# Kernel tuning notes

Hardware: AMD Instinct MI355X
Metric: run time of the kernel (lower is better)

The kernel has to match this reference:

```python
import jax, jax.numpy as jnp
import numpy as np

DYADIC_ORDER = 1
SIGMA = 1.0  # RBF static kernel bandwidth (concrete static_kernel for the abstract base)


def static_kernel(x, y):
    # RBF Gram matrix: K[i, j] = exp(-||x_i - y_j||^2 / (2 * sigma^2)); x:(Lx,d) y:(Ly,d)
    sq = (jnp.sum(x * x, axis=-1)[:, None]
          + jnp.sum(y * y, axis=-1)[None, :]
          - 2.0 * (x @ y.T))
    return jnp.exp(-sq / (2.0 * SIGMA ** 2))


def finite_diff(K, dyadic_order):
    # second mixed finite difference of the static kernel, refined on a dyadic grid
    diff = K[1:, 1:] + K[:-1, :-1] - K[1:, :-1] - K[:-1, 1:]
    n = 2 ** dyadic_order
    diff = jnp.repeat(jnp.repeat(diff, n, axis=0), n, axis=1) / float(n * n)
    return diff  # ((Lx-1)*n, (Ly-1)*n)


def solve_pde_final(A):
    """Solve the Goursat PDE recurrence on a (M+1, N+1) grid with boundary 1,
    k11 = (k10 + k01) * (1 + inc/2 + inc^2/12) - k00 * (1 - inc^2/12),
    via an anti-diagonal (wavefront) lax.scan. Returns K[M, N]."""
    M, N = A.shape
    # skew A so anti-diagonals become rows: Adiag[t, r] = A[r, t - r]
    t = jnp.arange(M + N - 1)[:, None]
    r = jnp.arange(M)[None, :]
    c = t - r
    Adiag = jnp.where((c >= 0) & (c < N), A[r, jnp.clip(c, 0, N - 1)], 0.0)

    ii = jnp.arange(M + 1)          # row index along a diagonal
    ones = jnp.ones(M + 1, A.dtype)
    ds = jnp.arange(2, M + N + 1)   # diagonal index d = i + j

    def step(carry, xs):
        prev2, prev1 = carry        # diagonals d-2, d-1 (entry i holds K[i, d'-i])
        Ad, d = xs
        zero = jnp.zeros((1,), A.dtype)
        inc = jnp.concatenate([zero, Ad])            # inc[i] = A[i-1, d-i-1]
        k10 = jnp.concatenate([zero, prev1[:-1]])    # K[i-1, j]
        k01 = prev1                                  # K[i, j-1]
        k00 = jnp.concatenate([zero, prev2[:-1]])    # K[i-1, j-1]
        k11 = (k10 + k01) * (1.0 + 0.5 * inc + inc * inc / 12.0) \
              - k00 * (1.0 - inc * inc / 12.0)
        jj = d - ii
        new = jnp.where((ii == 0) | (jj == 0), 1.0, k11)   # boundary condition = 1
        new = jnp.where((jj < 0) | (jj > N), 1.0, new)     # outside grid: keep inert
        return (prev1, new), None

    (_, last), _ = jax.lax.scan(step, (ones, ones), (Adiag, ds))
    return last[M]  # K[M, N] = pde_sol[-1, -1]


def sig_kernel_pair(x, y):
    K = static_kernel(x, y)
    A = finite_diff(K, DYADIC_ORDER)
    return solve_pde_final(A)


def batch_kernel(xs, ys):
    # xs: (Bx, Lx, d), ys: (By, Ly, d) -> (Bx, By) signature-kernel Gram matrix
    return jax.vmap(lambda x: jax.vmap(lambda y: sig_kernel_pair(x, y))(ys))(xs)


def setup_inputs() -> dict:
    key = jax.random.key(0)
    kx, ky = jax.random.split(key)
    xs = jax.random.normal(kx, (16, 128, 8), dtype=jnp.float32)
    ys = jax.random.normal(ky, (16, 128, 8), dtype=jnp.float32)
    return {"xs": xs, "ys": ys}


def reference(xs, ys):
    return batch_kernel(xs, ys)
```

## Files before the change

### kernel.cpp

```cpp
#include <hip/hip_runtime.h>


#define LX 128
#define D  8
#define NB 16
#define NBODY 190

__global__ __launch_bounds__(256)
void sigkernel_kernel(const float* __restrict__ xs,
                      const float* __restrict__ ys,
                      float* __restrict__ out)
{
    __shared__ float sx[LX][D + 1];
    __shared__ float sy[LX][D + 1];
    __shared__ float xsqv[LX];
    __shared__ float ysqv[LX];
    __shared__ float B[LX * LX];

    const int t  = threadIdx.x;
    const int bx = blockIdx.x;
    const int by = blockIdx.y;
    const float* xp = xs + bx * (LX * D);
    const float* yp = ys + by * (LX * D);

    for (int e = t; e < LX * D; e += 256) {
        sx[e >> 3][e & 7] = xp[e];
        sy[e >> 3][e & 7] = yp[e];
    }
    __syncthreads();

    if (t < LX) {
        float sxx = 0.f, syy = 0.f;
        #pragma unroll
        for (int k = 0; k < D; ++k) {
            sxx += sx[t][k] * sx[t][k];
            syy += sy[t][k] * sy[t][k];
        }
        xsqv[t] = sxx;
        ysqv[t] = syy;
    }
    __syncthreads();

    {
        const int j = t & 127;
        float yr[D];
        #pragma unroll
        for (int k = 0; k < D; ++k) yr[k] = sy[j][k];
        const float ysq = ysqv[j];
        #pragma unroll
        for (int c = 0; c < 64; ++c) {
            const int e = t + c * 256;
            const int i = e >> 7;
            float dot = 0.f;
            #pragma unroll
            for (int k = 0; k < D; ++k) dot += sx[i][k] * yr[k];
            const float sq = xsqv[i] + ysq - 2.0f * dot;
            B[e] = expf(-0.5f * sq);
        }
    }
    __syncthreads();

    {
        float rv[64];
        #pragma unroll
        for (int c = 0; c < 64; ++c) {
            const int idx = t + c * 256;
            if (idx < 127 * 127) {
                const int i = idx / 127;
                const int j = idx - i * 127;
                rv[c] = 0.25f * (B[(i + 1) * 128 + (j + 1)] + B[i * 128 + j]
                               - B[(i + 1) * 128 + j]       - B[i * 128 + (j + 1)]);
            }
        }
        __syncthreads();
        #pragma unroll
        for (int c = 0; c < 64; ++c) {
            const int idx = t + c * 256;
            if (idx < 127 * 127) {
                const int i = idx / 127;
                const int j = idx - i * 127;
                B[i * 128 + j] = rv[c];
            }
        }
        if (t < 127) B[t * 128 + 127] = 0.f;
    }
    __syncthreads();

    if (t >= 64) return;

    const int l = t;
    const int rowa = 2 * l;
    const int rowb = (2 * l + 1 > 126) ? 126 : 2 * l + 1;
    const int baseA = rowa * 128;
    const int baseB = rowb * 128;
    const bool lane0 = (l == 0);

    double cur0 = 1.0, cur1 = 1.0, cur2 = 1.0, cur3 = 1.0;
    double h0 = 1.0, h1 = 1.0, h2 = 1.0;

    float inA, inB;
    {
        const int q = -l;
        const bool cl = ((unsigned)q > 126u);
        inA = B[cl ? 127 : (baseA + q)];
        inB = B[cl ? 127 : (baseB + q)];
    }

    for (int k = 0; k < NBODY; ++k) {
        const double ia = (double)inA;
        const double ib = (double)inB;
        const double ea = ia * ia * (1.0 / 12.0);
        const double eb = ib * ib * (1.0 / 12.0);
        const double c1a = 1.0 + 0.5 * ia + ea, c2a = 1.0 - ea;
        const double c1b = 1.0 + 0.5 * ib + eb, c2b = 1.0 - eb;

        {
            const int qn = k + 1 - l;
            const bool cl = ((unsigned)qn > 126u);
            inA = B[cl ? 127 : (baseA + qn)];
            inB = B[cl ? 127 : (baseB + qn)];
        }

        #pragma unroll
        for (int sub = 0; sub < 2; ++sub) {
            const double k10 = lane0 ? 1.0 : h1;
            const double k00 = lane0 ? 1.0 : h2;
            const double n0 = (k10 + cur0) * c1a - k00  * c2a;
            const double n1 = (n0  + cur1) * c1a - cur0 * c2a;
            const double n2 = (n1  + cur2) * c1b - cur1 * c2b;
            const double n3 = (n2  + cur3) * c1b - cur2 * c2b;
            cur0 = n0; cur1 = n1; cur2 = n2; cur3 = n3;
            const double sh = __shfl_up(n3, 1);
            h2 = h1; h1 = h0; h0 = sh;
        }
    }

    if (l == 63) out[bx * NB + by] = (float)cur1;
}

extern "C" void kernel_launch(void* const* d_in, const int* in_sizes, int n_in,
                              void* d_out, int out_size, void* d_ws, size_t ws_size,
                              hipStream_t stream)
{
    const float* xs = (const float*)d_in[0];
    const float* ys = (const float*)d_in[1];
    float* out = (float*)d_out;
    dim3 grid(NB, NB);
    dim3 block(256);
    hipLaunchKernelGGL(sigkernel_kernel, grid, block, 0, stream, xs, ys, out);
}
```

Baseline: 89.48 us.

## Switch PDE wavefront recurrence to fp32 and simplify finite-difference indexing

Runs the serial Goursat wavefront recurrence in single precision instead of double. Fp64 work is replaced by fp32 FMAs, and each shuffle moves one 32-bit register instead of a 64-bit pair. The finite-difference pass now indexes linearly with a padded shared buffer, which removes the per-element divide by 127. The lane-0 boundary select moves into the shuffle update, and the main loop gets unroll 2. The cost is rounding error that builds up over about 380 serial steps, which could move the output away from the reference tolerance.

```diff
diff --git a/kernel.cpp b/kernel.cpp
--- a/kernel.cpp
+++ b/kernel.cpp
@@ -15,7 +15,7 @@
     __shared__ float sy[LX][D + 1];
     __shared__ float xsqv[LX];
     __shared__ float ysqv[LX];
-    __shared__ float B[LX * LX];
+    __shared__ float B[LX * LX + 132];
 
     const int t  = threadIdx.x;
     const int bx = blockIdx.x;
@@ -64,23 +64,15 @@
         float rv[64];
         #pragma unroll
         for (int c = 0; c < 64; ++c) {
-            const int idx = t + c * 256;
-            if (idx < 127 * 127) {
-                const int i = idx / 127;
-                const int j = idx - i * 127;
-                rv[c] = 0.25f * (B[(i + 1) * 128 + (j + 1)] + B[i * 128 + j]
-                               - B[(i + 1) * 128 + j]       - B[i * 128 + (j + 1)]);
-            }
+            const int e = t + c * 256;
+            rv[c] = 0.25f * (B[e + 129] + B[e] - B[e + 128] - B[e + 1]);
         }
         __syncthreads();
         #pragma unroll
         for (int c = 0; c < 64; ++c) {
-            const int idx = t + c * 256;
-            if (idx < 127 * 127) {
-                const int i = idx / 127;
-                const int j = idx - i * 127;
-                B[i * 128 + j] = rv[c];
-            }
+            const int e = t + c * 256;
+            const int i = e >> 7, j = e & 127;
+            if (i < 127 && j < 127) B[e] = rv[c];
         }
         if (t < 127) B[t * 128 + 127] = 0.f;
     }
@@ -95,8 +87,8 @@
     const int baseB = rowb * 128;
     const bool lane0 = (l == 0);
 
-    double cur0 = 1.0, cur1 = 1.0, cur2 = 1.0, cur3 = 1.0;
-    double h0 = 1.0, h1 = 1.0, h2 = 1.0;
+    float cur0 = 1.f, cur1 = 1.f, cur2 = 1.f, cur3 = 1.f;
+    float h0 = 1.f, h1 = 1.f, h2 = 1.f;
 
     float inA, inB;
     {
@@ -106,13 +98,14 @@
         inB = B[cl ? 127 : (baseB + q)];
     }
 
+    #pragma unroll 2
     for (int k = 0; k < NBODY; ++k) {
-        const double ia = (double)inA;
-        const double ib = (double)inB;
-        const double ea = ia * ia * (1.0 / 12.0);
-        const double eb = ib * ib * (1.0 / 12.0);
-        const double c1a = 1.0 + 0.5 * ia + ea, c2a = 1.0 - ea;
-        const double c1b = 1.0 + 0.5 * ib + eb, c2b = 1.0 - eb;
+        const float ia = inA;
+        const float ib = inB;
+        const float ea = ia * ia * (1.0f / 12.0f);
+        const float eb = ib * ib * (1.0f / 12.0f);
+        const float c1a = 1.0f + 0.5f * ia + ea, c2a = 1.0f - ea;
+        const float c1b = 1.0f + 0.5f * ib + eb, c2b = 1.0f - eb;
 
         {
             const int qn = k + 1 - l;
@@ -123,19 +116,17 @@
 
         #pragma unroll
         for (int sub = 0; sub < 2; ++sub) {
-            const double k10 = lane0 ? 1.0 : h1;
-            const double k00 = lane0 ? 1.0 : h2;
-            const double n0 = (k10 + cur0) * c1a - k00  * c2a;
-            const double n1 = (n0  + cur1) * c1a - cur0 * c2a;
-            const double n2 = (n1  + cur2) * c1b - cur1 * c2b;
-            const double n3 = (n2  + cur3) * c1b - cur2 * c2b;
+            const float n0 = (h1 + cur0) * c1a - h2   * c2a;
+            const float n1 = (n0 + cur1) * c1a - cur0 * c2a;
+            const float n2 = (n1 + cur2) * c1b - cur1 * c2b;
+            const float n3 = (n2 + cur3) * c1b - cur2 * c2b;
             cur0 = n0; cur1 = n1; cur2 = n2; cur3 = n3;
-            const double sh = __shfl_up(n3, 1);
-            h2 = h1; h1 = h0; h0 = sh;
+            const float sh = __shfl_up(n3, 1);
+            h2 = h1; h1 = h0; h0 = lane0 ? 1.0f : sh;
         }
     }
 
-    if (l == 63) out[bx * NB + by] = (float)cur1;
+    if (l == 63) out[bx * NB + by] = cur1;
 }
 
 extern "C" void kernel_launch(void* const* d_in, const int* in_sizes, int n_in,
```

New measurement: 91.37 us. 2.1% more time.
